# Performance work log

Measured on AMD Instinct MI355X. Metric: run time of the kernel, lower is better.

Reference implementation:

```python
import jax, jax.numpy as jnp
import numpy as np

# irrep multiplicities (match init_kwargs)
M0E, M1O, M1E, M0O = 64, 32, 32, 16
IN_DIM = M0E + 3 * M1O + 3 * M1E + M0O  # 272
# weight block shapes, in the fixed key order 0e, 1o, 1e, 0o
W_SHAPES = [("0e", M0E + M1O, M0E), ("1o", M0E + M1O + M1E, M1O), ("1e", M1O + M1E + M0O, M1E), ("0o", M1E + M0O, M0O)]
W_NUMEL = sum(a * b for _, a, b in W_SHAPES)  # 13568


def setup_inputs() -> dict:
    key = jax.random.key(0)
    k1, k2, k3 = jax.random.split(key, 3)
    B, N = 4, 128
    return {
        "in_": jax.random.normal(k1, (B, 1, N, IN_DIM), dtype=jnp.float32),
        "sh": jax.random.normal(k2, (B, N, 1, 4), dtype=jnp.float32),
        "weight": jax.random.normal(k3, (W_NUMEL,), dtype=jnp.float32),
    }


def _split_weights(weight):
    out, start = {}, 0
    for key, a, b in W_SHAPES:
        out[key] = weight[..., start:start + a * b].reshape(weight.shape[:-1] + (a, b)) / np.sqrt(a).astype(np.float32)
        start += a * b
    return out


def reference(in_, sh, weight):
    # split input irreps: [B,1,N,272] -> 0e [B,1,N,64], 1o [B,1,N,32,3], 1e [B,1,N,32,3], 0o [B,1,N,16]
    i = 0
    x0e = in_[..., i:i + M0E]; i += M0E
    x1o = in_[..., i:i + 3 * M1O].reshape(in_.shape[:-1] + (M1O, 3)); i += 3 * M1O
    x1e = in_[..., i:i + 3 * M1E].reshape(in_.shape[:-1] + (M1E, 3)); i += 3 * M1E
    x0o = in_[..., i:i + M0O]

    sh0 = sh[..., 0]          # [B,N,1]
    sh1 = sh[..., 1:]         # [B,N,1,3]
    sh1b = sh1[..., None, :]  # [B,N,1,1,3] (broadcast against mul axis)
    inv_s3 = np.float32(1.0 / np.sqrt(3.0))
    inv_s2 = np.float32(1.0 / np.sqrt(2.0))

    # pairwise broadcast: [B,1,N,...] x [B,N,1,...] -> [B,N,N,...]
    out0e = jnp.concatenate([
        x0e * sh0[..., None],                       # [B,N,N,64]
        (x1o * sh1b).sum(-1) * inv_s3,              # [B,N,N,32]
    ], axis=-1)                                     # [B,N,N,96]

    out1o = jnp.concatenate([
        x0e[..., None] * sh1b,                      # [B,N,N,64,3]
        x1o * sh0[..., None, None],                 # [B,N,N,32,3]
        jnp.cross(x1e, sh1b) * inv_s2,              # [B,N,N,32,3]
    ], axis=-2)                                     # [B,N,N,128,3]

    out1e = jnp.concatenate([
        jnp.cross(x1o, sh1b) * inv_s2,              # [B,N,N,32,3]
        x1e * sh0[..., None, None],                 # [B,N,N,32,3]
        x0o[..., None] * sh1b,                      # [B,N,N,16,3]
    ], axis=-2)                                     # [B,N,N,80,3]

    out0o = jnp.concatenate([
        (x1e * sh1b).sum(-1) * inv_s3,              # [B,N,N,32]
        x0o * sh0[..., None],                       # [B,N,N,16]
    ], axis=-1)                                     # [B,N,N,48]

    W = _split_weights(weight)
    y0e = out0e @ W["0e"]                                            # [B,N,N,64]
    y1o = jnp.einsum("bnmkc,ko->bnmoc", out1o, W["1o"])             # [B,N,N,32,3]
    y1o = y1o.reshape(y1o.shape[:-2] + (-1,))                        # [B,N,N,96]
    y1e = jnp.einsum("bnmkc,ko->bnmoc", out1e, W["1e"])             # [B,N,N,32,3]
    y1e = y1e.reshape(y1e.shape[:-2] + (-1,))                        # [B,N,N,96]
    y0o = out0o @ W["0o"]                                            # [B,N,N,16]

    # out_irreps order: 64x0e + 32x1o + 32x1e + 16x0o
    return jnp.concatenate([y0e, y1o, y1e, y0o], axis=-1)            # [B,N,N,272]
```

## Files before the change

### kernel.cpp

```cpp
#include <hip/hip_runtime.h>


constexpr float INV_S3 = 0.57735026918962576f;
constexpr float INV_S2 = 0.70710678118654752f;
constexpr float SC0E = 0.10206207261596577f;
constexpr float SC1O = 0.08838834764831845f;
constexpr float SC1E = 0.11180339887498949f;
constexpr float SC0O = 0.14433756729740643f;

#define P0E 97
#define P1O 129
#define P1E 81
#define P0O 49

__global__ __launch_bounds__(320) void stage_a(const float* __restrict__ in_,
                                               const float* __restrict__ weight,
                                               float* __restrict__ Z) {
    __shared__ float xs[272];
    __shared__ float o0e[4 * P0E];
    __shared__ float o1oT[12 * P1O];
    __shared__ float o1eT[12 * P1E];
    __shared__ float o0o[4 * P0O];

    const int tid = threadIdx.x;
    const int row = blockIdx.x;
    const float* x = in_ + row * 272;

    if (tid < 68) ((float4*)xs)[tid] = ((const float4*)x)[tid];
    __syncthreads();

    for (int idx = tid; idx < 4 * 96; idx += 320) {
        int c = idx / 96, k = idx - c * 96;
        float v = 0.f;
        if (k < 64) { if (c == 0) v = xs[k]; }
        else        { if (c >= 1) v = xs[64 + (k - 64) * 3 + (c - 1)] * INV_S3; }
        o0e[c * P0E + k] = v * SC0E;
    }
    for (int idx = tid; idx < 4 * 3 * 128; idx += 320) {
        int c = idx / 384, rem = idx - c * 384, d = rem >> 7, k = rem & 127;
        float v = 0.f;
        if (k < 64) {
            if (c >= 1 && d == c - 1) v = xs[k];
        } else if (k < 96) {
            if (c == 0) v = xs[64 + (k - 64) * 3 + d];
        } else {
            if (c >= 1) {
                int t = c - 1, j = k - 96;
                float a1 = xs[160 + j * 3 + (d + 1) % 3];
                float a2 = xs[160 + j * 3 + (d + 2) % 3];
                v = ((((d + 2) % 3) == t) ? a1 : 0.f) - ((((d + 1) % 3) == t) ? a2 : 0.f);
                v *= INV_S2;
            }
        }
        o1oT[(c * 3 + d) * P1O + k] = v * SC1O;
    }
    for (int idx = tid; idx < 4 * 3 * 80; idx += 320) {
        int c = idx / 240, rem = idx - c * 240, d = rem / 80, k = rem - d * 80;
        float v = 0.f;
        if (k < 32) {
            if (c >= 1) {
                int t = c - 1;
                float a1 = xs[64 + k * 3 + (d + 1) % 3];
                float a2 = xs[64 + k * 3 + (d + 2) % 3];
                v = ((((d + 2) % 3) == t) ? a1 : 0.f) - ((((d + 1) % 3) == t) ? a2 : 0.f);
                v *= INV_S2;
            }
        } else if (k < 64) {
            if (c == 0) v = xs[160 + (k - 32) * 3 + d];
        } else {
            if (c >= 1 && d == c - 1) v = xs[256 + (k - 64)];
        }
        o1eT[(c * 3 + d) * P1E + k] = v * SC1E;
    }
    for (int idx = tid; idx < 4 * 48; idx += 320) {
        int c = idx / 48, k = idx - c * 48;
        float v = 0.f;
        if (k < 32) { if (c >= 1) v = xs[160 + k * 3 + (c - 1)] * INV_S3; }
        else        { if (c == 0) v = xs[256 + (k - 32)]; }
        o0o[c * P0O + k] = v * SC0O;
    }
    __syncthreads();

    float* zrow = Z + row * 1088;

    if (tid < 64) {
        int c = tid >> 4, o4 = tid & 15;
        const float* wp = weight + o4 * 4;
        const float* op = o0e + c * P0E;
        float ax = 0.f, ay = 0.f, az = 0.f, aw = 0.f;
        #pragma unroll 8
        for (int k = 0; k < 96; ++k) {
            float s = op[k];
            float4 w = *(const float4*)(wp + k * 64);
            ax += s * w.x; ay += s * w.y; az += s * w.z; aw += s * w.w;
        }
        float4 r; r.x = ax; r.y = ay; r.z = az; r.w = aw;
        *(float4*)(zrow + c * 272 + o4 * 4) = r;
    } else if (tid < 160) {
        int t2 = tid - 64;
        int c = t2 / 24, r2 = t2 - c * 24, d = r2 >> 3, o4 = r2 & 7;
        const float* wp = weight + 6144 + o4 * 4;
        const float* op = o1oT + (c * 3 + d) * P1O;
        float ax = 0.f, ay = 0.f, az = 0.f, aw = 0.f;
        #pragma unroll 8
        for (int k = 0; k < 128; ++k) {
            float s = op[k];
            float4 w = *(const float4*)(wp + k * 32);
            ax += s * w.x; ay += s * w.y; az += s * w.z; aw += s * w.w;
        }
        float* zb = zrow + c * 272 + 64 + d;
        zb[(o4 * 4 + 0) * 3] = ax;
        zb[(o4 * 4 + 1) * 3] = ay;
        zb[(o4 * 4 + 2) * 3] = az;
        zb[(o4 * 4 + 3) * 3] = aw;
    } else if (tid < 256) {
        int t2 = tid - 160;
        int c = t2 / 24, r2 = t2 - c * 24, d = r2 >> 3, o4 = r2 & 7;
        const float* wp = weight + 10240 + o4 * 4;
        const float* op = o1eT + (c * 3 + d) * P1E;
        float ax = 0.f, ay = 0.f, az = 0.f, aw = 0.f;
        #pragma unroll 8
        for (int k = 0; k < 80; ++k) {
            float s = op[k];
            float4 w = *(const float4*)(wp + k * 32);
            ax += s * w.x; ay += s * w.y; az += s * w.z; aw += s * w.w;
        }
        float* zb = zrow + c * 272 + 160 + d;
        zb[(o4 * 4 + 0) * 3] = ax;
        zb[(o4 * 4 + 1) * 3] = ay;
        zb[(o4 * 4 + 2) * 3] = az;
        zb[(o4 * 4 + 3) * 3] = aw;
    } else if (tid < 272) {
        int t2 = tid - 256;
        int c = t2 >> 2, o4 = t2 & 3;
        const float* wp = weight + 12800 + o4 * 4;
        const float* op = o0o + c * P0O;
        float ax = 0.f, ay = 0.f, az = 0.f, aw = 0.f;
        #pragma unroll 8
        for (int k = 0; k < 48; ++k) {
            float s = op[k];
            float4 w = *(const float4*)(wp + k * 16);
            ax += s * w.x; ay += s * w.y; az += s * w.z; aw += s * w.w;
        }
        float4 r; r.x = ax; r.y = ay; r.z = az; r.w = aw;
        *(float4*)(zrow + c * 272 + 256 + o4 * 4) = r;
    }
}

__global__ __launch_bounds__(256) void stage_b(const float4* __restrict__ Z4,
                                               const float* __restrict__ sh,
                                               float4* __restrict__ out4) {
    __shared__ float shs[64];
    const int tid = threadIdx.x;
    int blk = blockIdx.x;
    int b = blk / 272;
    int rem = blk - b * 272;
    int mch = rem / 34;
    int pblk = rem - mch * 34;
    int p = pblk * 256 + tid;
    int n = p / 68;
    int o4 = p - n * 68;
    int m0 = mch * 16;

    if (tid < 64) shs[tid] = sh[(b * 128 + m0) * 4 + tid];
    __syncthreads();

    const float4* zr = Z4 + (size_t)((b * 128 + n) * 4) * 68 + o4;
    float4 z0 = zr[0];
    float4 z1 = zr[68];
    float4 z2 = zr[2 * 68];
    float4 z3 = zr[3 * 68];

    float4* ob = out4 + (size_t)(b * 128 + m0) * 8704 + p;
    #pragma unroll 4
    for (int j = 0; j < 16; ++j) {
        float s0 = shs[j * 4 + 0];
        float s1 = shs[j * 4 + 1];
        float s2 = shs[j * 4 + 2];
        float s3 = shs[j * 4 + 3];
        float4 v;
        v.x = s0 * z0.x + s1 * z1.x + s2 * z2.x + s3 * z3.x;
        v.y = s0 * z0.y + s1 * z1.y + s2 * z2.y + s3 * z3.y;
        v.z = s0 * z0.z + s1 * z1.z + s2 * z2.z + s3 * z3.z;
        v.w = s0 * z0.w + s1 * z1.w + s2 * z2.w + s3 * z3.w;
        ob[(size_t)j * 8704] = v;
    }
}

extern "C" void kernel_launch(void* const* d_in, const int* in_sizes, int n_in,
                              void* d_out, int out_size, void* d_ws, size_t ws_size,
                              hipStream_t stream) {
    (void)in_sizes; (void)n_in; (void)out_size; (void)ws_size;
    const float* in_ = (const float*)d_in[0];
    const float* sh  = (const float*)d_in[1];
    const float* w   = (const float*)d_in[2];
    float* Z = (float*)d_ws;
    float* out = (float*)d_out;

    stage_a<<<512, 320, 0, stream>>>(in_, w, Z);
    stage_b<<<1088, 256, 0, stream>>>((const float4*)Z, sh, (float4*)out);
}
```

Baseline: 99.80 us.

## Flatten stage_b to one output float4 per thread, dropping per-block m loop

Stage_b now launches one thread per output float4 (17408 blocks) instead of each thread writing 16 m-rows. The shared-memory staging of sh and its barrier are removed, and each thread reads its sh float4 directly. This raises parallelism for the write-bound broadcast. In exchange, the Z row loads are no longer reused across 16 outputs, so Z is re-read roughly 16x more, though mostly from cache.

```diff
diff --git a/kernel.cpp b/kernel.cpp
--- a/kernel.cpp
+++ b/kernel.cpp
@@ -148,43 +148,28 @@
 }
 
 __global__ __launch_bounds__(256) void stage_b(const float4* __restrict__ Z4,
-                                               const float* __restrict__ sh,
+                                               const float4* __restrict__ sh4,
                                                float4* __restrict__ out4) {
-    __shared__ float shs[64];
-    const int tid = threadIdx.x;
-    int blk = blockIdx.x;
-    int b = blk / 272;
-    int rem = blk - b * 272;
-    int mch = rem / 34;
-    int pblk = rem - mch * 34;
-    int p = pblk * 256 + tid;
-    int n = p / 68;
+    int g = blockIdx.x * 256 + threadIdx.x;
+    int bm = g / 8704;
+    int p  = g - bm * 8704;
+    int n  = p / 68;
     int o4 = p - n * 68;
-    int m0 = mch * 16;
+    int b  = bm >> 7;
 
-    if (tid < 64) shs[tid] = sh[(b * 128 + m0) * 4 + tid];
-    __syncthreads();
-
+    float4 s = sh4[bm];
     const float4* zr = Z4 + (size_t)((b * 128 + n) * 4) * 68 + o4;
     float4 z0 = zr[0];
     float4 z1 = zr[68];
     float4 z2 = zr[2 * 68];
     float4 z3 = zr[3 * 68];
 
-    float4* ob = out4 + (size_t)(b * 128 + m0) * 8704 + p;
-    #pragma unroll 4
-    for (int j = 0; j < 16; ++j) {
-        float s0 = shs[j * 4 + 0];
-        float s1 = shs[j * 4 + 1];
-        float s2 = shs[j * 4 + 2];
-        float s3 = shs[j * 4 + 3];
-        float4 v;
-        v.x = s0 * z0.x + s1 * z1.x + s2 * z2.x + s3 * z3.x;
-        v.y = s0 * z0.y + s1 * z1.y + s2 * z2.y + s3 * z3.y;
-        v.z = s0 * z0.z + s1 * z1.z + s2 * z2.z + s3 * z3.z;
-        v.w = s0 * z0.w + s1 * z1.w + s2 * z2.w + s3 * z3.w;
-        ob[(size_t)j * 8704] = v;
-    }
+    float4 v;
+    v.x = s.x * z0.x + s.y * z1.x + s.z * z2.x + s.w * z3.x;
+    v.y = s.x * z0.y + s.y * z1.y + s.z * z2.y + s.w * z3.y;
+    v.z = s.x * z0.z + s.y * z1.z + s.z * z2.z + s.w * z3.z;
+    v.w = s.x * z0.w + s.y * z1.w + s.z * z2.w + s.w * z3.w;
+    out4[g] = v;
 }
 
 extern "C" void kernel_launch(void* const* d_in, const int* in_sizes, int n_in,
@@ -198,5 +183,5 @@
     float* out = (float*)d_out;
 
     stage_a<<<512, 320, 0, stream>>>(in_, w, Z);
-    stage_b<<<1088, 256, 0, stream>>>((const float4*)Z, sh, (float4*)out);
+    stage_b<<<17408, 256, 0, stream>>>((const float4*)Z, (const float4*)sh, (float4*)out);
 }
```

After: 104.3 us. 1.04x slower.
